# Performance work log

Measured on AMD Instinct MI355X. Metric: run time of the kernel, lower is better.

The kernel has to match this reference:

```python
import jax, jax.numpy as jnp
import numpy as np

HIDDEN = 512
HORIZON = 24
IN = 2


def _lstm_cell(xproj, h, c, Whh, bhh):
    # xproj: [B,4H] precomputed input projection (incl. b_ih)
    gates = xproj + h @ Whh.T + bhh
    i, f, g, o = jnp.split(gates, 4, axis=-1)  # PyTorch gate order: i,f,g,o
    i = jax.nn.sigmoid(i)
    f = jax.nn.sigmoid(f)
    g = jnp.tanh(g)
    o = jax.nn.sigmoid(o)
    c = f * c + i * g
    h = o * jnp.tanh(c)
    return h, c


def _run_lstm_layer(x_tbd, Wih, bih, Whh, bhh):
    # x_tbd: [T,B,D_in] -> outputs [T,B,H], final (h,c)
    xp = x_tbd @ Wih.T + bih  # one big GEMM for input projections
    B = x_tbd.shape[1]
    h0 = jnp.zeros((B, HIDDEN), x_tbd.dtype)
    c0 = jnp.zeros((B, HIDDEN), x_tbd.dtype)

    def step(carry, xt):
        h, c = carry
        h, c = _lstm_cell(xt, h, c, Whh, bhh)
        return (h, c), h

    (h, c), hs = jax.lax.scan(step, (h0, c0), xp)
    return hs, h, c


def setup_inputs() -> dict:
    key = jax.random.key(0)
    ks = jax.random.split(key, 32)
    s = 0.05
    H = HIDDEN
    d = {"x": jax.random.normal(ks[0], (512, 128, IN), jnp.float32)}
    shapes = {
        "enc_Wih0": (4 * H, IN), "enc_Whh0": (4 * H, H), "enc_bih0": (4 * H,), "enc_bhh0": (4 * H,),
        "enc_Wih1": (4 * H, H), "enc_Whh1": (4 * H, H), "enc_bih1": (4 * H,), "enc_bhh1": (4 * H,),
        "dec_Wih0": (4 * H, IN), "dec_Whh0": (4 * H, H), "dec_bih0": (4 * H,), "dec_bhh0": (4 * H,),
        "dec_Wih1": (4 * H, H), "dec_Whh1": (4 * H, H), "dec_bih1": (4 * H,), "dec_bhh1": (4 * H,),
        "fc_W": (IN, H), "fc_b": (IN,),
    }
    for i, (name, shp) in enumerate(shapes.items()):
        d[name] = jax.random.normal(ks[i + 1], shp, jnp.float32) * s
    return d


def reference(x,
              enc_Wih0, enc_Whh0, enc_bih0, enc_bhh0,
              enc_Wih1, enc_Whh1, enc_bih1, enc_bhh1,
              dec_Wih0, dec_Whh0, dec_bih0, dec_bhh0,
              dec_Wih1, dec_Whh1, dec_bih1, dec_bhh1,
              fc_W, fc_b):
    B = x.shape[0]
    x_tbd = jnp.transpose(x, (1, 0, 2))  # [T,B,2]
    # Encoder: 2-layer LSTM (eval mode -> no dropout)
    hs1, h1, c1 = _run_lstm_layer(x_tbd, enc_Wih0, enc_bih0, enc_Whh0, enc_bhh0)
    _, h2, c2 = _run_lstm_layer(hs1, enc_Wih1, enc_bih1, enc_Whh1, enc_bhh1)

    dec_in0 = jnp.zeros((B, IN), x.dtype)

    def dec_step(carry, _):
        dec_in, dh1, dc1, dh2, dc2 = carry
        xp1 = dec_in @ dec_Wih0.T + dec_bih0
        dh1, dc1 = _lstm_cell(xp1, dh1, dc1, dec_Whh0, dec_bhh0)
        xp2 = dh1 @ dec_Wih1.T + dec_bih1
        dh2, dc2 = _lstm_cell(xp2, dh2, dc2, dec_Whh1, dec_bhh1)
        pred = dh2 @ fc_W.T + fc_b  # [B,2]
        return (pred, dh1, dc1, dh2, dc2), pred

    # decoder initial state = encoder final state (layer-wise)
    _, preds = jax.lax.scan(dec_step, (dec_in0, h1, c1, h2, c2), None, length=HORIZON)
    return jnp.transpose(preds, (1, 0, 2))  # [B,horizon,2]
```

## Files before the change

### kernel.cpp

```cpp
#include <hip/hip_runtime.h>
#include <hip/hip_bf16.h>
#include <math.h>
#include <stdint.h>

#define HID 512
#define NB  512
#define TT  128
#define HOR 24
#define G4  2048
#define SLOT (512*512)

typedef __attribute__((ext_vector_type(8))) short bf16x8;
typedef __attribute__((ext_vector_type(4))) float f32x4;

#define FL(a, s, gg) ((a) + (((s) * 8 + (gg)) << 4))

#define WAITB(n) asm volatile("s_waitcnt vmcnt(" #n ")\ns_barrier" ::: "memory")

struct PK {
  const float* x;
  const __hip_bfloat16 *W0r, *W1c, *Wd0c, *Wd1c;
  const float *b0r, *b1r, *bd0s0, *bd0r, *bd1r, *Wx0r;
  const float *fcW, *fcb;
  __hip_bfloat16 *h0buf, *h1buf, *dh1buf, *dh2buf;
  const __hip_bfloat16* zbuf;
  int *f0, *f1, *fd1, *fd2;
  float* out;
};

__device__ __forceinline__ void gl_lds16(void* lds, const void* g) {
  __builtin_amdgcn_global_load_lds((const __attribute__((address_space(1))) void*)g,
                                   (__attribute__((address_space(3))) void*)lds, 16, 0, 0);
}

__device__ __forceinline__ float sigm(float x) { return 1.0f / (1.0f + expf(-x)); }

__device__ __forceinline__ void waitflag_nb(int* f) {
  if (threadIdx.x == 0) {
    while (__hip_atomic_load(f, __ATOMIC_RELAXED, __HIP_MEMORY_SCOPE_AGENT) < 32)
      __builtin_amdgcn_s_sleep(1);
  }
  asm volatile("s_barrier" ::: "memory");
}

__device__ __forceinline__ void arrive(int* f) {
  __syncthreads();
  if (threadIdx.x == 0)
    __hip_atomic_fetch_add(f, 1, __ATOMIC_RELAXED, __HIP_MEMORY_SCOPE_AGENT);
}

template<int KC>
__device__ __forceinline__ void load_w(bf16x8* Breg, const __hip_bfloat16* W,
                                       int Kt, int nrow, int q) {
  const char* base = (const char*)W + ((size_t)nrow * Kt + q * 8) * 2;
#pragma unroll
  for (int kc = 0; kc < KC; ++kc)
    Breg[kc] = *(const bf16x8*)(base + (size_t)kc * 64);
}

__device__ __forceinline__ void stage_chunk(const __hip_bfloat16* As, int c,
                                            char* dst, int goff, int tid) {
  const __hip_bfloat16* base = As + ((size_t)(goff + c) << 13);
#pragma unroll
  for (int i = 0; i < 4; ++i) {
    const int u = (i << 8) + tid;
    gl_lds16(dst + (size_t)u * 16, base + ((size_t)u << 3));
  }
}

__device__ __forceinline__ void mfma_chunk(const char* sA, const bf16x8* Breg, int bb,
                                           int q, int s, f32x4* acc) {
#pragma unroll
  for (int kl = 0; kl < 4; ++kl) {
#pragma unroll
    for (int mi = 0; mi < 4; ++mi) {
      bf16x8 a = *(const bf16x8*)(sA +
          (size_t)((((kl << 2) + q) << 6) + (mi << 4) + s) * 16);
      acc[mi] = __builtin_amdgcn_mfma_f32_16x16x32_bf16(a, Breg[bb + kl], acc[mi], 0, 0, 0);
    }
  }
}

__device__ __forceinline__ void gemm4(const __hip_bfloat16* Af, const bf16x8* Breg,
                                      int goff, char* smem, int lane, f32x4* acc) {
  const int tid = threadIdx.x;
  const int s = lane & 15, q = lane >> 4;
#pragma unroll
  for (int mi = 0; mi < 4; ++mi) acc[mi] = (f32x4){0.f, 0.f, 0.f, 0.f};
  stage_chunk(Af, 0, smem,         goff, tid);
  stage_chunk(Af, 1, smem + 16384, goff, tid);
  stage_chunk(Af, 2, smem + 32768, goff, tid);
  WAITB(8); stage_chunk(Af, 3, smem + 49152, goff, tid);
            mfma_chunk(smem,         Breg, 0,  q, s, acc);
  WAITB(8); mfma_chunk(smem + 16384, Breg, 4,  q, s, acc);
  WAITB(4); mfma_chunk(smem + 32768, Breg, 8,  q, s, acc);
  WAITB(0); mfma_chunk(smem + 49152, Breg, 12, q, s, acc);
}

__device__ __forceinline__ void gemm8(
    const __hip_bfloat16* Af, int bo1,
    const __hip_bfloat16* As2, int bo2, int* f2,
    const bf16x8* Breg, int goff, char* smem, int lane, f32x4* acc) {
  const int tid = threadIdx.x;
  const int s = lane & 15, q = lane >> 4;
#pragma unroll
  for (int mi = 0; mi < 4; ++mi) acc[mi] = (f32x4){0.f, 0.f, 0.f, 0.f};
  stage_chunk(Af, 0, smem,         goff, tid);
  stage_chunk(Af, 1, smem + 16384, goff, tid);
  stage_chunk(Af, 2, smem + 32768, goff, tid);
  WAITB(8); stage_chunk(Af, 3, smem + 49152, goff, tid);
            mfma_chunk(smem,         Breg, bo1 + 0,  q, s, acc);
  WAITB(8); mfma_chunk(smem + 16384, Breg, bo1 + 4,  q, s, acc);
  WAITB(4);
  if (f2) waitflag_nb(f2);
  stage_chunk(As2, 0, smem,         goff, tid);
  stage_chunk(As2, 1, smem + 16384, goff, tid);
            mfma_chunk(smem + 32768, Breg, bo1 + 8,  q, s, acc);
  WAITB(8); stage_chunk(As2, 2, smem + 32768, goff, tid);
            mfma_chunk(smem + 49152, Breg, bo1 + 12, q, s, acc);
  WAITB(8); stage_chunk(As2, 3, smem + 49152, goff, tid);
            mfma_chunk(smem,         Breg, bo2 + 0,  q, s, acc);
  WAITB(8); mfma_chunk(smem + 16384, Breg, bo2 + 4,  q, s, acc);
  WAITB(4); mfma_chunk(smem + 32768, Breg, bo2 + 8,  q, s, acc);
  WAITB(0); mfma_chunk(smem + 49152, Breg, bo2 + 12, q, s, acc);
}

__device__ __forceinline__ void epilogue(
    const f32x4* __restrict__ acc, float* __restrict__ tbuf, ushort* __restrict__ hsh,
    const f32x4 bz, const f32x4* w01, const f32x4* w23, const float2* xr,
    float* __restrict__ creg, __hip_bfloat16* __restrict__ hout,
    int hoff, int lane) {
  const int s = lane & 15, q = lane >> 4;
  const int row_e = lane >> 2, jl = lane & 3;
#pragma unroll
  for (int mi = 0; mi < 4; ++mi) {
#pragma unroll
    for (int r = 0; r < 4; ++r)
      tbuf[mi * 320 + (q * 4 + r) * 20 + s] = acc[mi][r];
  }
#pragma unroll
  for (int mi = 0; mi < 4; ++mi) {
    f32x4 gv = *(const f32x4*)&tbuf[mi * 320 + row_e * 20 + jl * 4];
    float gi = gv[0] + bz[0], gf = gv[1] + bz[1];
    float gg = gv[2] + bz[2], go = gv[3] + bz[3];
    if (xr) {
      gi += xr[mi].x * (*w01)[0] + xr[mi].y * (*w01)[1];
      gf += xr[mi].x * (*w01)[2] + xr[mi].y * (*w01)[3];
      gg += xr[mi].x * (*w23)[0] + xr[mi].y * (*w23)[1];
      go += xr[mi].x * (*w23)[2] + xr[mi].y * (*w23)[3];
    }
    float iv = sigm(gi), fv = sigm(gf), gvv = tanhf(gg), ov = sigm(go);
    float cv = fv * creg[mi] + iv * gvv;
    creg[mi] = cv;
    __hip_bfloat16 hv = __float2bfloat16(ov * tanhf(cv));
    hsh[(mi << 6) + lane] = __builtin_bit_cast(unsigned short, hv);
  }
  unsigned long long pk;
  asm volatile("" ::: "memory");
  __builtin_memcpy(&pk, &hsh[lane << 2], 8);
  __hip_atomic_store((unsigned long long*)(hout + hoff),
                     pk, __ATOMIC_RELAXED, __HIP_MEMORY_SCOPE_AGENT);
}

__device__ __forceinline__ void pred_job2(const __hip_bfloat16* h2, const float* fcW,
                                          const float* fcb, float* outp,
                                          int d2, int g, int nt) {
  const int wv = threadIdx.x >> 6, lane = threadIdx.x & 63;
  if (wv < 2) {
    const int bl = nt * 2 + wv;
    const int b = g * 64 + bl;
    float s0 = 0.f, s1 = 0.f;
    for (int k = lane; k < 512; k += 64) {
      const int unit = ((g * 4 + (k >> 7)) * 16 + ((k >> 3) & 15)) * 64 + bl;
      float hv = __bfloat162float(h2[(size_t)unit * 8 + (k & 7)]);
      s0 += hv * fcW[k];
      s1 += hv * fcW[512 + k];
    }
    for (int off = 32; off; off >>= 1) {
      s0 += __shfl_down(s0, off);
      s1 += __shfl_down(s1, off);
    }
    if (lane == 0) {
      outp[(size_t)b * (HOR * 2) + d2 * 2]     = s0 + fcb[0];
      outp[(size_t)b * (HOR * 2) + d2 * 2 + 1] = s1 + fcb[1];
    }
  }
}

__global__ __launch_bounds__(256, 2) void seq2seq_persistent(PK p) {
  __shared__ __align__(16) char smem[65536];
  const int blk = blockIdx.x;
  const int g = blk & 7;
  const int role = (blk >> 3) & 1;
  const int nt = blk >> 4;
  const int goff = g * 4;
  const int wv = threadIdx.x >> 6, lane = threadIdx.x & 63;
  const int s16 = lane & 15, q = lane >> 4;
  const int nrow = nt * 64 + wv * 16 + s16;
  const int jg = nt * 16 + wv * 4 + (lane & 3);
  const int n4 = jg * 4;
  const int hoff = (((goff + (nt >> 3)) * 16 + ((2 * nt + (wv >> 1)) & 15)) * 64 + lane) * 8
                   + (wv & 1) * 4;
  float* tbuf = (float*)(smem) + wv * 1280;
  ushort* hsh = (ushort*)(smem + 20480) + wv * 256;

  f32x4 acc[4];
  bf16x8 Breg[32];
  float creg[4] = {0.f, 0.f, 0.f, 0.f};

  if (role == 1) {
    load_w<32>(Breg, p.W1c, 1024, nrow, q);
    f32x4 bz = *(const f32x4*)&p.b1r[n4];
    for (int u = 0; u < TT; ++u) {
      waitflag_nb(FL(p.f0, u, g));
      const __hip_bfloat16* A2 = (u == 0) ? p.zbuf : p.h1buf + (size_t)(u - 1) * SLOT;
      int* f2 = (u == 0) ? nullptr : FL(p.f1, u - 1, g);
      gemm8(p.h0buf + (size_t)u * SLOT, 0, A2, 16, f2, Breg, goff, smem, lane, acc);
      epilogue(acc, tbuf, hsh, bz, nullptr, nullptr, nullptr, creg,
               p.h1buf + (size_t)u * SLOT, hoff, lane);
      arrive(FL(p.f1, u, g));
    }
    load_w<32>(Breg, p.Wd1c, 1024, nrow, q);
    bz = *(const f32x4*)&p.bd1r[n4];
    for (int d = 0; d < HOR; ++d) {
      if (d == 0) waitflag_nb(FL(p.f1, 127, g));
      else        waitflag_nb(FL(p.fd2, d - 1, g));
      const __hip_bfloat16* Af = (d == 0) ? p.h1buf + (size_t)127 * SLOT
                                          : p.dh2buf + (size_t)(d - 1) * SLOT;
      gemm8(Af, 16, p.dh1buf + (size_t)d * SLOT, 0, FL(p.fd1, d, g),
            Breg, goff, smem, lane, acc);
      epilogue(acc, tbuf, hsh, bz, nullptr, nullptr, nullptr, creg,
               p.dh2buf + (size_t)d * SLOT, hoff, lane);
      arrive(FL(p.fd2, d, g));
    }
  } else {
    load_w<16>(Breg, p.W0r, 512, nrow, q);
    f32x4 bz = *(const f32x4*)&p.b0r[n4];
    f32x4 w01 = *(const f32x4*)&p.Wx0r[n4 * 2];
    f32x4 w23 = *(const f32x4*)&p.Wx0r[n4 * 2 + 4];
    const int row_e = lane >> 2;
    const int m0 = g * 64;
    for (int s = 0; s < TT; ++s) {
      if (s >= 1) waitflag_nb(FL(p.f0, s - 1, g));
      gemm4((s == 0) ? p.zbuf : p.h0buf + (size_t)(s - 1) * SLOT,
            Breg, goff, smem, lane, acc);
      float2 xr[4];
#pragma unroll
      for (int mi = 0; mi < 4; ++mi)
        xr[mi] = *(const float2*)&p.x[((size_t)(m0 + mi * 16 + row_e) * TT + s) * 2];
      epilogue(acc, tbuf, hsh, bz, &w01, &w23, xr, creg,
               p.h0buf + (size_t)s * SLOT, hoff, lane);
      arrive(FL(p.f0, s, g));
    }
    load_w<32>(Breg, p.Wd0c, 1024, nrow, q);
    f32x4 bzd0 = *(const f32x4*)&p.bd0s0[n4];
    f32x4 bzd  = *(const f32x4*)&p.bd0r[n4];
    for (int d = 0; d < HOR; ++d) {
      const __hip_bfloat16 *Af, *As2; int* f2; f32x4 bzu;
      if (d == 0) {
        waitflag_nb(FL(p.f0, 127, g));
        Af = p.h0buf + (size_t)127 * SLOT; As2 = p.zbuf; f2 = nullptr; bzu = bzd0;
      } else {
        waitflag_nb(FL(p.fd1, d - 1, g));
        Af  = p.dh1buf + (size_t)(d - 1) * SLOT;
        As2 = p.dh2buf + (size_t)(d - 1) * SLOT;
        f2 = FL(p.fd2, d - 1, g); bzu = bzd;
      }
      gemm8(Af, 0, As2, 16, f2, Breg, goff, smem, lane, acc);
      epilogue(acc, tbuf, hsh, bzu, nullptr, nullptr, nullptr, creg,
               p.dh1buf + (size_t)d * SLOT, hoff, lane);
      arrive(FL(p.fd1, d, g));
      if (d >= 1)
        pred_job2(p.dh2buf + (size_t)(d - 1) * SLOT, p.fcW, p.fcb, p.out, d - 1, g, nt);
    }
    waitflag_nb(FL(p.fd2, 23, g));
    pred_job2(p.dh2buf + (size_t)23 * SLOT, p.fcW, p.fcb, p.out, 23, g, nt);
  }
}

__global__ void prep_weights(
    const float* eWih0, const float* eWhh0, const float* ebih0, const float* ebhh0,
    const float* eWih1, const float* eWhh1, const float* ebih1, const float* ebhh1,
    const float* dWih0, const float* dWhh0, const float* dbih0, const float* dbhh0,
    const float* dWih1, const float* dWhh1, const float* dbih1, const float* dbhh1,
    const float* fcW, const float* fcb,
    __hip_bfloat16* W0r, __hip_bfloat16* W1c, __hip_bfloat16* Wd0c, __hip_bfloat16* Wd1c,
    float* b0r, float* b1r, float* bd0s0, float* bd0r, float* bd1r, float* Wx0r) {
  long idx = (long)blockIdx.x * blockDim.x + threadIdx.x;
  if (idx >= (long)G4 * 3584) return;
  int np = (int)(idx / 3584), kk = (int)(idx % 3584);
  int g = np & 3, j = np >> 2;
  int srow = g * HID + j;
  if (kk < 512) {
    W0r[(size_t)np * 512 + kk] = __float2bfloat16(eWhh0[(size_t)srow * 512 + kk]);
  } else if (kk < 1536) {
    int k2 = kk - 512;
    float v = (k2 < 512) ? eWih1[(size_t)srow * 512 + k2] : eWhh1[(size_t)srow * 512 + (k2 - 512)];
    W1c[(size_t)np * 1024 + k2] = __float2bfloat16(v);
  } else if (kk < 2560) {
    int k2 = kk - 1536;
    float v;
    if (k2 < 512) v = dWhh0[(size_t)srow * 512 + k2];
    else {
      int k3 = k2 - 512;
      v = dWih0[srow * 2] * fcW[k3] + dWih0[srow * 2 + 1] * fcW[512 + k3];
    }
    Wd0c[(size_t)np * 1024 + k2] = __float2bfloat16(v);
  } else {
    int k2 = kk - 2560;
    float v = (k2 < 512) ? dWih1[(size_t)srow * 512 + k2] : dWhh1[(size_t)srow * 512 + (k2 - 512)];
    Wd1c[(size_t)np * 1024 + k2] = __float2bfloat16(v);
  }
  if (kk == 0) {
    b0r[np] = ebih0[srow] + ebhh0[srow];
    b1r[np] = ebih1[srow] + ebhh1[srow];
    float bs0 = dbih0[srow] + dbhh0[srow];
    bd0s0[np] = bs0;
    bd0r[np] = bs0 + dWih0[srow * 2] * fcb[0] + dWih0[srow * 2 + 1] * fcb[1];
    bd1r[np] = dbih1[srow] + dbhh1[srow];
    Wx0r[np * 2]     = eWih0[srow * 2];
    Wx0r[np * 2 + 1] = eWih0[srow * 2 + 1];
  }
}

extern "C" void kernel_launch(void* const* d_in, const int* in_sizes, int n_in,
                              void* d_out, int out_size, void* d_ws, size_t ws_size,
                              hipStream_t stream) {
  (void)in_sizes; (void)n_in; (void)out_size; (void)ws_size;
  const float* x     = (const float*)d_in[0];
  const float* eWih0 = (const float*)d_in[1];
  const float* eWhh0 = (const float*)d_in[2];
  const float* ebih0 = (const float*)d_in[3];
  const float* ebhh0 = (const float*)d_in[4];
  const float* eWih1 = (const float*)d_in[5];
  const float* eWhh1 = (const float*)d_in[6];
  const float* ebih1 = (const float*)d_in[7];
  const float* ebhh1 = (const float*)d_in[8];
  const float* dWih0 = (const float*)d_in[9];
  const float* dWhh0 = (const float*)d_in[10];
  const float* dbih0 = (const float*)d_in[11];
  const float* dbhh0 = (const float*)d_in[12];
  const float* dWih1 = (const float*)d_in[13];
  const float* dWhh1 = (const float*)d_in[14];
  const float* dbih1 = (const float*)d_in[15];
  const float* dbhh1 = (const float*)d_in[16];
  const float* fcW   = (const float*)d_in[17];
  const float* fcb   = (const float*)d_in[18];

  char* ws = (char*)d_ws;
  size_t off = 0;
  auto alloc = [&](size_t bytes) -> char* {
    char* pp = ws + off;
    off = (off + bytes + 255) & ~(size_t)255;
    return pp;
  };

  __hip_bfloat16* W0r  = (__hip_bfloat16*)alloc((size_t)G4 * 512 * 2);
  __hip_bfloat16* W1c  = (__hip_bfloat16*)alloc((size_t)G4 * 1024 * 2);
  __hip_bfloat16* Wd0c = (__hip_bfloat16*)alloc((size_t)G4 * 1024 * 2);
  __hip_bfloat16* Wd1c = (__hip_bfloat16*)alloc((size_t)G4 * 1024 * 2);
  float* b0r   = (float*)alloc(G4 * 4);
  float* b1r   = (float*)alloc(G4 * 4);
  float* bd0s0 = (float*)alloc(G4 * 4);
  float* bd0r  = (float*)alloc(G4 * 4);
  float* bd1r  = (float*)alloc(G4 * 4);
  float* Wx0r  = (float*)alloc(G4 * 2 * 4);

  __hip_bfloat16* h0buf  = (__hip_bfloat16*)alloc((size_t)TT * SLOT * 2);
  __hip_bfloat16* h1buf  = (__hip_bfloat16*)alloc((size_t)TT * SLOT * 2);
  __hip_bfloat16* dh1buf = (__hip_bfloat16*)alloc((size_t)HOR * SLOT * 2);
  __hip_bfloat16* dh2buf = (__hip_bfloat16*)alloc((size_t)HOR * SLOT * 2);

  char* zbase = ws + off;
  __hip_bfloat16* zbuf = (__hip_bfloat16*)alloc((size_t)SLOT * 2);
  int* f0  = (int*)alloc(TT * 8 * 16 * 4);
  int* f1  = (int*)alloc(TT * 8 * 16 * 4);
  int* fd1 = (int*)alloc(HOR * 8 * 16 * 4);
  int* fd2 = (int*)alloc(HOR * 8 * 16 * 4);
  size_t zbytes = (size_t)((ws + off) - zbase);

  hipMemsetAsync(zbase, 0, zbytes, stream);
  prep_weights<<<(int)(((long)G4 * 3584 + 255) / 256), 256, 0, stream>>>(
      eWih0, eWhh0, ebih0, ebhh0, eWih1, eWhh1, ebih1, ebhh1,
      dWih0, dWhh0, dbih0, dbhh0, dWih1, dWhh1, dbih1, dbhh1,
      fcW, fcb, W0r, W1c, Wd0c, Wd1c, b0r, b1r, bd0s0, bd0r, bd1r, Wx0r);

  PK p;
  p.x = x;
  p.W0r = W0r; p.W1c = W1c; p.Wd0c = Wd0c; p.Wd1c = Wd1c;
  p.b0r = b0r; p.b1r = b1r; p.bd0s0 = bd0s0; p.bd0r = bd0r; p.bd1r = bd1r; p.Wx0r = Wx0r;
  p.fcW = fcW; p.fcb = fcb;
  p.h0buf = h0buf; p.h1buf = h1buf; p.dh1buf = dh1buf; p.dh2buf = dh2buf;
  p.zbuf = zbuf;
  p.f0 = f0; p.f1 = f1; p.fd1 = fd1; p.fd2 = fd2;
  p.out = (float*)d_out;

  seq2seq_persistent<<<512, 256, 0, stream>>>(p);
}
```

Measured before the change: 1.317 ms.

## Use fast activations, per-wave flag polling, vectorized fc prediction, earlier x loads

Swaps the libm sigmoid and tanh for __expf plus hardware reciprocal approximations. Changes the flag wait so the first lane of each wave polls on its own, with no block barrier. Rewrites the fc prediction to use one 16-byte load per lane against a pre-permuted fc weight array built in a new prep kernel. Hoists the x loads ahead of the layer-0 GEMM. These aim to cut transcendental cost, barrier stalls and scattered loads on the serial recurrence path, at the cost of slightly lower activation precision and heavier per-wave polling traffic.

```diff
diff --git a/kernel.cpp b/kernel.cpp
--- a/kernel.cpp
+++ b/kernel.cpp
@@ -21,7 +21,7 @@
   const float* x;
   const __hip_bfloat16 *W0r, *W1c, *Wd0c, *Wd1c;
   const float *b0r, *b1r, *bd0s0, *bd0r, *bd1r, *Wx0r;
-  const float *fcW, *fcb;
+  const float *fcWr, *fcb;
   __hip_bfloat16 *h0buf, *h1buf, *dh1buf, *dh2buf;
   const __hip_bfloat16* zbuf;
   int *f0, *f1, *fd1, *fd2;
@@ -33,14 +33,19 @@
                                    (__attribute__((address_space(3))) void*)lds, 16, 0, 0);
 }
 
-__device__ __forceinline__ float sigm(float x) { return 1.0f / (1.0f + expf(-x)); }
-
-__device__ __forceinline__ void waitflag_nb(int* f) {
-  if (threadIdx.x == 0) {
+__device__ __forceinline__ float fsigm(float x) {
+  return __builtin_amdgcn_rcpf(1.f + __expf(-x));
+}
+__device__ __forceinline__ float ftanh(float x) {
+  return 2.f * __builtin_amdgcn_rcpf(1.f + __expf(-2.f * x)) - 1.f;
+}
+
+__device__ __forceinline__ void waitflag_w(int* f) {
+  if ((threadIdx.x & 63) == 0) {
     while (__hip_atomic_load(f, __ATOMIC_RELAXED, __HIP_MEMORY_SCOPE_AGENT) < 32)
       __builtin_amdgcn_s_sleep(1);
   }
-  asm volatile("s_barrier" ::: "memory");
+  asm volatile("" ::: "memory");
 }
 
 __device__ __forceinline__ void arrive(int* f) {
@@ -112,7 +117,7 @@
             mfma_chunk(smem,         Breg, bo1 + 0,  q, s, acc);
   WAITB(8); mfma_chunk(smem + 16384, Breg, bo1 + 4,  q, s, acc);
   WAITB(4);
-  if (f2) waitflag_nb(f2);
+  if (f2) waitflag_w(f2);
   stage_chunk(As2, 0, smem,         goff, tid);
   stage_chunk(As2, 1, smem + 16384, goff, tid);
             mfma_chunk(smem + 32768, Breg, bo1 + 8,  q, s, acc);
@@ -149,10 +154,10 @@
       gg += xr[mi].x * (*w23)[0] + xr[mi].y * (*w23)[1];
       go += xr[mi].x * (*w23)[2] + xr[mi].y * (*w23)[3];
     }
-    float iv = sigm(gi), fv = sigm(gf), gvv = tanhf(gg), ov = sigm(go);
+    float iv = fsigm(gi), fv = fsigm(gf), gvv = ftanh(gg), ov = fsigm(go);
     float cv = fv * creg[mi] + iv * gvv;
     creg[mi] = cv;
-    __hip_bfloat16 hv = __float2bfloat16(ov * tanhf(cv));
+    __hip_bfloat16 hv = __float2bfloat16(ov * ftanh(cv));
     hsh[(mi << 6) + lane] = __builtin_bit_cast(unsigned short, hv);
   }
   unsigned long long pk;
@@ -162,28 +167,29 @@
                      pk, __ATOMIC_RELAXED, __HIP_MEMORY_SCOPE_AGENT);
 }
 
-__device__ __forceinline__ void pred_job2(const __hip_bfloat16* h2, const float* fcW,
+__device__ __forceinline__ void pred_fast(const __hip_bfloat16* h2, const float* fcWr,
                                           const float* fcb, float* outp,
                                           int d2, int g, int nt) {
   const int wv = threadIdx.x >> 6, lane = threadIdx.x & 63;
-  if (wv < 2) {
-    const int bl = nt * 2 + wv;
-    const int b = g * 64 + bl;
-    float s0 = 0.f, s1 = 0.f;
-    for (int k = lane; k < 512; k += 64) {
-      const int unit = ((g * 4 + (k >> 7)) * 16 + ((k >> 3) & 15)) * 64 + bl;
-      float hv = __bfloat162float(h2[(size_t)unit * 8 + (k & 7)]);
-      s0 += hv * fcW[k];
-      s1 += hv * fcW[512 + k];
-    }
-    for (int off = 32; off; off >>= 1) {
-      s0 += __shfl_down(s0, off);
-      s1 += __shfl_down(s1, off);
-    }
-    if (lane == 0) {
-      outp[(size_t)b * (HOR * 2) + d2 * 2]     = s0 + fcb[0];
-      outp[(size_t)b * (HOR * 2) + d2 * 2 + 1] = s1 + fcb[1];
-    }
+  if (wv >= 2) return;
+  const int bl = nt * 2 + wv, b = g * 64 + bl;
+  const size_t unit = (size_t)(g * 4 + (lane >> 4)) * 1024 + (size_t)((lane & 15) * 64 + bl);
+  unsigned short us[8];
+  __builtin_memcpy(us, h2 + unit * 8, 16);
+  float s0 = 0.f, s1 = 0.f;
+#pragma unroll
+  for (int e = 0; e < 8; ++e) {
+    float hv = __builtin_bit_cast(float, (unsigned)us[e] << 16);
+    s0 += hv * fcWr[lane * 8 + e];
+    s1 += hv * fcWr[512 + lane * 8 + e];
+  }
+  for (int off = 32; off; off >>= 1) {
+    s0 += __shfl_down(s0, off);
+    s1 += __shfl_down(s1, off);
+  }
+  if (lane == 0) {
+    outp[(size_t)b * (HOR * 2) + d2 * 2]     = s0 + fcb[0];
+    outp[(size_t)b * (HOR * 2) + d2 * 2 + 1] = s1 + fcb[1];
   }
 }
 
@@ -197,8 +203,7 @@
   const int wv = threadIdx.x >> 6, lane = threadIdx.x & 63;
   const int s16 = lane & 15, q = lane >> 4;
   const int nrow = nt * 64 + wv * 16 + s16;
-  const int jg = nt * 16 + wv * 4 + (lane & 3);
-  const int n4 = jg * 4;
+  const int n4 = (nt * 16 + wv * 4 + (lane & 3)) * 4;
   const int hoff = (((goff + (nt >> 3)) * 16 + ((2 * nt + (wv >> 1)) & 15)) * 64 + lane) * 8
                    + (wv & 1) * 4;
   float* tbuf = (float*)(smem) + wv * 1280;
@@ -212,7 +217,7 @@
     load_w<32>(Breg, p.W1c, 1024, nrow, q);
     f32x4 bz = *(const f32x4*)&p.b1r[n4];
     for (int u = 0; u < TT; ++u) {
-      waitflag_nb(FL(p.f0, u, g));
+      waitflag_w(FL(p.f0, u, g));
       const __hip_bfloat16* A2 = (u == 0) ? p.zbuf : p.h1buf + (size_t)(u - 1) * SLOT;
       int* f2 = (u == 0) ? nullptr : FL(p.f1, u - 1, g);
       gemm8(p.h0buf + (size_t)u * SLOT, 0, A2, 16, f2, Breg, goff, smem, lane, acc);
@@ -223,8 +228,8 @@
     load_w<32>(Breg, p.Wd1c, 1024, nrow, q);
     bz = *(const f32x4*)&p.bd1r[n4];
     for (int d = 0; d < HOR; ++d) {
-      if (d == 0) waitflag_nb(FL(p.f1, 127, g));
-      else        waitflag_nb(FL(p.fd2, d - 1, g));
+      if (d == 0) waitflag_w(FL(p.f1, 127, g));
+      else        waitflag_w(FL(p.fd2, d - 1, g));
       const __hip_bfloat16* Af = (d == 0) ? p.h1buf + (size_t)127 * SLOT
                                           : p.dh2buf + (size_t)(d - 1) * SLOT;
       gemm8(Af, 16, p.dh1buf + (size_t)d * SLOT, 0, FL(p.fd1, d, g),
@@ -241,13 +246,13 @@
     const int row_e = lane >> 2;
     const int m0 = g * 64;
     for (int s = 0; s < TT; ++s) {
-      if (s >= 1) waitflag_nb(FL(p.f0, s - 1, g));
+      if (s >= 1) waitflag_w(FL(p.f0, s - 1, g));
+      float2 xr[4];
+#pragma unroll
+      for (int mi = 0; mi < 4; ++mi)
+        xr[mi] = *(const float2*)&p.x[((size_t)(m0 + mi * 16 + row_e) * TT + s) * 2];
       gemm4((s == 0) ? p.zbuf : p.h0buf + (size_t)(s - 1) * SLOT,
             Breg, goff, smem, lane, acc);
-      float2 xr[4];
-#pragma unroll
-      for (int mi = 0; mi < 4; ++mi)
-        xr[mi] = *(const float2*)&p.x[((size_t)(m0 + mi * 16 + row_e) * TT + s) * 2];
       epilogue(acc, tbuf, hsh, bz, &w01, &w23, xr, creg,
                p.h0buf + (size_t)s * SLOT, hoff, lane);
       arrive(FL(p.f0, s, g));
@@ -258,10 +263,10 @@
     for (int d = 0; d < HOR; ++d) {
       const __hip_bfloat16 *Af, *As2; int* f2; f32x4 bzu;
       if (d == 0) {
-        waitflag_nb(FL(p.f0, 127, g));
+        waitflag_w(FL(p.f0, 127, g));
         Af = p.h0buf + (size_t)127 * SLOT; As2 = p.zbuf; f2 = nullptr; bzu = bzd0;
       } else {
-        waitflag_nb(FL(p.fd1, d - 1, g));
+        waitflag_w(FL(p.fd1, d - 1, g));
         Af  = p.dh1buf + (size_t)(d - 1) * SLOT;
         As2 = p.dh2buf + (size_t)(d - 1) * SLOT;
         f2 = FL(p.fd2, d - 1, g); bzu = bzd;
@@ -271,10 +276,10 @@
                p.dh1buf + (size_t)d * SLOT, hoff, lane);
       arrive(FL(p.fd1, d, g));
       if (d >= 1)
-        pred_job2(p.dh2buf + (size_t)(d - 1) * SLOT, p.fcW, p.fcb, p.out, d - 1, g, nt);
-    }
-    waitflag_nb(FL(p.fd2, 23, g));
-    pred_job2(p.dh2buf + (size_t)23 * SLOT, p.fcW, p.fcb, p.out, 23, g, nt);
+        pred_fast(p.dh2buf + (size_t)(d - 1) * SLOT, p.fcWr, p.fcb, p.out, d - 1, g, nt);
+    }
+    waitflag_w(FL(p.fd2, 23, g));
+    pred_fast(p.dh2buf + (size_t)23 * SLOT, p.fcWr, p.fcb, p.out, 23, g, nt);
   }
 }
 
@@ -323,6 +328,15 @@
   }
 }
 
+__global__ void prep_fcw(const float* fcW, float* fcWr) {
+  int t = blockIdx.x * blockDim.x + threadIdx.x;
+  if (t >= 1024) return;
+  int r = t >> 9, j = t & 511;
+  int l = j >> 3, e = j & 7;
+  int k = ((l >> 4) << 7) + ((l & 15) << 3) + e;
+  fcWr[t] = fcW[r * 512 + k];
+}
+
 extern "C" void kernel_launch(void* const* d_in, const int* in_sizes, int n_in,
                               void* d_out, int out_size, void* d_ws, size_t ws_size,
                               hipStream_t stream) {
@@ -365,6 +379,7 @@
   float* bd0r  = (float*)alloc(G4 * 4);
   float* bd1r  = (float*)alloc(G4 * 4);
   float* Wx0r  = (float*)alloc(G4 * 2 * 4);
+  float* fcWr  = (float*)alloc(1024 * 4);
 
   __hip_bfloat16* h0buf  = (__hip_bfloat16*)alloc((size_t)TT * SLOT * 2);
   __hip_bfloat16* h1buf  = (__hip_bfloat16*)alloc((size_t)TT * SLOT * 2);
@@ -384,12 +399,13 @@
       eWih0, eWhh0, ebih0, ebhh0, eWih1, eWhh1, ebih1, ebhh1,
       dWih0, dWhh0, dbih0, dbhh0, dWih1, dWhh1, dbih1, dbhh1,
       fcW, fcb, W0r, W1c, Wd0c, Wd1c, b0r, b1r, bd0s0, bd0r, bd1r, Wx0r);
+  prep_fcw<<<4, 256, 0, stream>>>(fcW, fcWr);
 
   PK p;
   p.x = x;
   p.W0r = W0r; p.W1c = W1c; p.Wd0c = Wd0c; p.Wd1c = Wd1c;
   p.b0r = b0r; p.b1r = b1r; p.bd0s0 = bd0s0; p.bd0r = bd0r; p.bd1r = bd1r; p.Wx0r = Wx0r;
-  p.fcW = fcW; p.fcb = fcb;
+  p.fcWr = fcWr; p.fcb = fcb;
   p.h0buf = h0buf; p.h1buf = h1buf; p.dh1buf = dh1buf; p.dh2buf = dh2buf;
   p.zbuf = zbuf;
   p.f0 = f0; p.f1 = f1; p.fd1 = fd1; p.fd2 = fd2;
```

New measurement: 1.379 ms. 4.8% more time.
